# Kernel tuning notes

Measured on AMD Instinct MI355X. Metric: run time of the kernel, lower is better.

Reference implementation:

```python
import jax, jax.numpy as jnp
import numpy as np

# VAR block scales (x,y,z) -> per-scale token counts x*y*z
BLOCK_SCALES = [(1,1,1),(2,2,1),(3,3,1),(4,4,1),(5,5,1),(6,6,1),(8,8,1),(10,10,1),(13,13,1),(16,16,1)]
LENGTHS = [x*y*z for x, y, z in BLOCK_SCALES]  # [1,4,9,...,256], sum = 680
L = int(np.sum(LENGTHS))
B, H, D = 8, 16, 64


def _var_mask():
    # document_id[i] = which scale block token i belongs to
    doc = np.repeat(np.arange(len(LENGTHS), dtype=np.int32), LENGTHS)  # [L]
    idx = np.arange(L)
    same_doc = doc[:, None] == doc[None, :]
    causal = idx[:, None] >= idx[None, :]
    return jnp.asarray(same_doc | causal)  # [L, L] bool


MASK = _var_mask()


def setup_inputs() -> dict:
    key = jax.random.key(0)
    kq, kk, kv = jax.random.split(key, 3)
    q = jax.random.normal(kq, (B, H, L, D), dtype=jnp.float32)
    k = jax.random.normal(kk, (B, H, L, D), dtype=jnp.float32)
    v = jax.random.normal(kv, (B, H, L, D), dtype=jnp.float32)
    return {"q": q, "k": k, "v": v}


def reference(q, k, v):
    # flex_attention default scale = 1/sqrt(head_dim)
    scale = 1.0 / np.sqrt(D).astype(np.float32)
    scores = jnp.einsum("bhqd,bhkd->bhqk", q, k) * scale  # [B,H,L,L]
    neg = jnp.asarray(jnp.finfo(scores.dtype).min, scores.dtype)
    scores = jnp.where(MASK, scores, neg)
    attn = jax.nn.softmax(scores, axis=-1)
    return jnp.einsum("bhqk,bhkd->bhqd", attn, v)
```

## Files before the change

kernel.cpp:

```cpp
#include <hip/hip_runtime.h>


typedef float  f32x4 __attribute__((ext_vector_type(4)));
typedef short  s16x8 __attribute__((ext_vector_type(8)));
typedef unsigned int u32;
typedef u32    u32x4 __attribute__((ext_vector_type(4)));

#define L_TOK 680
#define DHEAD 64
#define NBH   128
#define SCALE_LOG2 0.18033688011112042f

__device__ __forceinline__ int kv_len(int q) {
  return q < 1 ? 1 : q < 5 ? 5 : q < 14 ? 14 : q < 30 ? 30 : q < 55 ? 55
       : q < 91 ? 91 : q < 155 ? 155 : q < 255 ? 255 : q < 424 ? 424 : L_TOK;
}

__device__ __forceinline__ short f2bf(float x) {
  unsigned u = __float_as_uint(x);
  return (short)((u + 0x7FFFu + ((u >> 16) & 1u)) >> 16);
}

__device__ __forceinline__ s16x8 cvt8(f32x4 a, f32x4 b, float sc) {
  s16x8 f;
  f[0] = f2bf(a[0] * sc); f[1] = f2bf(a[1] * sc);
  f[2] = f2bf(a[2] * sc); f[3] = f2bf(a[3] * sc);
  f[4] = f2bf(b[0] * sc); f[5] = f2bf(b[1] * sc);
  f[6] = f2bf(b[2] * sc); f[7] = f2bf(b[3] * sc);
  return f;
}

__device__ __forceinline__ float exp2f_raw(float x) {
  float r; asm("v_exp_f32 %0, %1" : "=v"(r) : "v"(x)); return r;
}
__device__ __forceinline__ u32 cvtpk(float lo, float hi) {
  u32 r; asm("v_cvt_pk_bf16_f32 %0, %1, %2" : "=v"(r) : "v"(lo), "v"(hi)); return r;
}

__global__ __launch_bounds__(512, 4) void var_attn14(
    const float* __restrict__ Qg, const float* __restrict__ Kg,
    const float* __restrict__ Vg, float* __restrict__ Og)
{
  const int tid  = threadIdx.x;
  const int lane = tid & 63, wave = tid >> 6;
  const int l15  = lane & 15, lg = lane >> 4;

  int bid  = blockIdx.x;
  int bhlo = bid & 7;
  int t_   = bid >> 3;
  int qbi  = t_ >> 4;
  int bhhi = t_ & 15;
  int qb2  = (qbi < 3) ? (qbi + 3) : (5 - qbi);
  int bh   = bhhi * 8 + bhlo;
  int qblk = qb2 * 128;

  __shared__ short kbuf[3][64 * DHEAD];
  __shared__ short vbuf[3][64 * DHEAD];

  const int qw        = qblk + wave * 16;
  const int qc        = min(qw + l15, L_TOK - 1);
  const int my_kvlen  = kv_len(qc);
  const int kvmin_w   = kv_len(min(qw, L_TOK - 1));
  const int kv_need_w = (qw < L_TOK) ? kv_len(min(qw + 15, L_TOK - 1)) : 0;
  const int nkv       = kv_len(min(qblk + 127, L_TOK - 1));
  const int nt        = (nkv + 63) >> 6;

  s16x8 qfrag[2];
  {
    const float* qp = Qg + ((size_t)(bh * L_TOK + qc)) * DHEAD + lg * 8;
    #pragma unroll
    for (int ks = 0; ks < 2; ++ks) {
      f32x4 a = *(const f32x4*)(qp + ks * 32);
      f32x4 b = *(const f32x4*)(qp + ks * 32 + 4);
      qfrag[ks] = cvt8(a, b, SCALE_LOG2);
    }
  }

  const float* kbase = Kg + (size_t)bh * L_TOK * DHEAD;
  const float* vbase = Vg + (size_t)bh * L_TOK * DHEAD;

  const int kr_s = tid >> 3, kc_s = tid & 7;
  const int vd_s = tid & 63, lg_s = (tid >> 6) & 3, f_s = tid >> 8;

  f32x4 kA, kB;
  float vA[8];

  auto loadregs = [&](int kt) {
    const int kv0 = kt * 64;
    const float* kp = kbase + (size_t)min(kv0 + kr_s, L_TOK - 1) * DHEAD + kc_s * 8;
    kA = *(const f32x4*)kp;
    kB = *(const f32x4*)(kp + 4);
    #pragma unroll
    for (int i = 0; i < 4; ++i) {
      int kv  = kv0 + f_s * 32 + lg_s * 4 + i;
      vA[i]     = vbase[(size_t)min(kv,      L_TOK - 1) * DHEAD + vd_s];
      vA[4 + i] = vbase[(size_t)min(kv + 16, L_TOK - 1) * DHEAD + vd_s];
    }
  };

  auto writelds = [&](int buf) {
    u32x4 kw;
    kw[0] = cvtpk(kA[0], kA[1]); kw[1] = cvtpk(kA[2], kA[3]);
    kw[2] = cvtpk(kB[0], kB[1]); kw[3] = cvtpk(kB[2], kB[3]);
    *(u32x4*)(&kbuf[buf][kr_s * 64 + ((kc_s ^ (kr_s & 7)) * 8)]) = kw;
    u32x4 vw;
    vw[0] = cvtpk(vA[0], vA[1]); vw[1] = cvtpk(vA[2], vA[3]);
    vw[2] = cvtpk(vA[4], vA[5]); vw[3] = cvtpk(vA[6], vA[7]);
    int pos = (2 * lg_s + f_s) ^ (vd_s & 7);
    *(u32x4*)(&vbuf[buf][vd_s * 64 + pos * 8]) = vw;
  };

  const int swz   = l15 & 7;
  const int koff0 = l15 * 128 + ((lg    ) ^ swz) * 16;
  const int koff1 = l15 * 128 + ((lg + 4) ^ swz) * 16;
  const int voff0 = l15 * 128 + ((2 * lg    ) ^ swz) * 16;
  const int voff1 = l15 * 128 + ((2 * lg + 1) ^ swz) * 16;

  f32x4 oacc[4] = {};
  float l_run = 0.0f;

  loadregs(0);
  writelds(0);
  __syncthreads();

  int bcur = 0;
  for (int kt = 0; kt < nt; ++kt) {
    if (kt + 1 < nt) loadregs(kt + 1);

    const int kv0 = kt * 64;
    if (kv0 < kv_need_w) {
      const char* kb = (const char*)&kbuf[bcur][0];
      const char* vb = (const char*)&vbuf[bcur][0];

      f32x4 sacc[4] = {};
      __builtin_amdgcn_s_setprio(1);
      #pragma unroll
      for (int t16 = 0; t16 < 4; ++t16) {
        s16x8 kf0 = *(const s16x8*)(kb + t16 * 2048 + koff0);
        s16x8 kf1 = *(const s16x8*)(kb + t16 * 2048 + koff1);
        sacc[t16] = __builtin_amdgcn_mfma_f32_16x16x32_bf16(kf0, qfrag[0], sacc[t16], 0, 0, 0);
        sacc[t16] = __builtin_amdgcn_mfma_f32_16x16x32_bf16(kf1, qfrag[1], sacc[t16], 0, 0, 0);
      }
      __builtin_amdgcn_s_setprio(0);

      u32x4 w0, w1;
      float lsum = 0.0f;
      if (kv0 + 64 <= kvmin_w) {
        #pragma unroll
        for (int t16 = 0; t16 < 4; ++t16) {
          float a = exp2f_raw(sacc[t16][0]);
          float b = exp2f_raw(sacc[t16][1]);
          float c = exp2f_raw(sacc[t16][2]);
          float d = exp2f_raw(sacc[t16][3]);
          lsum += (a + b) + (c + d);
          u32 lo = cvtpk(a, b), hi = cvtpk(c, d);
          if (t16 < 2) { w0[2 * t16] = lo; w0[2 * t16 + 1] = hi; }
          else         { w1[2 * (t16 - 2)] = lo; w1[2 * (t16 - 2) + 1] = hi; }
        }
      } else {
        const int kbq = kv0 + lg * 4;
        #pragma unroll
        for (int t16 = 0; t16 < 4; ++t16) {
          float a = (kbq + t16 * 16     < my_kvlen) ? exp2f_raw(sacc[t16][0]) : 0.0f;
          float b = (kbq + t16 * 16 + 1 < my_kvlen) ? exp2f_raw(sacc[t16][1]) : 0.0f;
          float c = (kbq + t16 * 16 + 2 < my_kvlen) ? exp2f_raw(sacc[t16][2]) : 0.0f;
          float d = (kbq + t16 * 16 + 3 < my_kvlen) ? exp2f_raw(sacc[t16][3]) : 0.0f;
          lsum += (a + b) + (c + d);
          u32 lo = cvtpk(a, b), hi = cvtpk(c, d);
          if (t16 < 2) { w0[2 * t16] = lo; w0[2 * t16 + 1] = hi; }
          else         { w1[2 * (t16 - 2)] = lo; w1[2 * (t16 - 2) + 1] = hi; }
        }
      }
      l_run += lsum;
      s16x8 pf0 = __builtin_bit_cast(s16x8, w0);
      s16x8 pf1 = __builtin_bit_cast(s16x8, w1);

      __builtin_amdgcn_s_setprio(1);
      #pragma unroll
      for (int dt = 0; dt < 4; ++dt) {
        s16x8 vf0 = *(const s16x8*)(vb + dt * 2048 + voff0);
        s16x8 vf1 = *(const s16x8*)(vb + dt * 2048 + voff1);
        oacc[dt] = __builtin_amdgcn_mfma_f32_16x16x32_bf16(pf0, vf0, oacc[dt], 0, 0, 0);
        oacc[dt] = __builtin_amdgcn_mfma_f32_16x16x32_bf16(pf1, vf1, oacc[dt], 0, 0, 0);
      }
      __builtin_amdgcn_s_setprio(0);
    }

    if (kt + 1 < nt) {
      int bnext = (bcur == 2) ? 0 : bcur + 1;
      writelds(bnext);
      __syncthreads();
      bcur = bnext;
    }
  }

  l_run += __shfl_xor(l_run, 16);
  l_run += __shfl_xor(l_run, 32);
  float linv = 1.0f / l_run;
  float li_q[4];
  #pragma unroll
  for (int r = 0; r < 4; ++r) li_q[r] = __shfl(linv, lg * 4 + r);
  #pragma unroll
  for (int r = 0; r < 4; ++r) {
    int qo = qw + lg * 4 + r;
    if (qo < L_TOK) {
      float* dst = Og + ((size_t)(bh * L_TOK + qo)) * DHEAD + l15;
      #pragma unroll
      for (int dt = 0; dt < 4; ++dt) dst[dt * 16] = oacc[dt][r] * li_q[r];
    }
  }
}

extern "C" void kernel_launch(void* const* d_in, const int* in_sizes, int n_in,
                              void* d_out, int out_size, void* d_ws, size_t ws_size,
                              hipStream_t stream) {
  const float* q = (const float*)d_in[0];
  const float* k = (const float*)d_in[1];
  const float* v = (const float*)d_in[2];
  float* o = (float*)d_out;
  (void)d_ws; (void)ws_size;
  var_attn14<<<768, 512, 0, stream>>>(q, k, v, o);
}
```

Baseline: 33.16 us.

## Process two 16-row query tiles per wave with 256-thread blocks

Each wave now handles 32 query rows as two 16-row MFMA tiles that share every K and V fragment read from LDS, halving LDS reads per query. The block shrinks from 8 to 4 waves while still covering 128 queries, so each thread stages twice as much K/V into shared memory per tile. This trades lower LDS traffic and fewer waves competing for the barrier against more registers per thread, fewer waves per block, and less latency hiding.

```diff
diff --git a/kernel.cpp b/kernel.cpp
--- a/kernel.cpp
+++ b/kernel.cpp
@@ -37,7 +37,7 @@
   u32 r; asm("v_cvt_pk_bf16_f32 %0, %1, %2" : "=v"(r) : "v"(lo), "v"(hi)); return r;
 }
 
-__global__ __launch_bounds__(512, 4) void var_attn14(
+__global__ __launch_bounds__(256, 3) void var_attn15(
     const float* __restrict__ Qg, const float* __restrict__ Kg,
     const float* __restrict__ Vg, float* __restrict__ Og)
 {
@@ -57,57 +57,72 @@
   __shared__ short kbuf[3][64 * DHEAD];
   __shared__ short vbuf[3][64 * DHEAD];
 
-  const int qw        = qblk + wave * 16;
-  const int qc        = min(qw + l15, L_TOK - 1);
-  const int my_kvlen  = kv_len(qc);
+  const int qw        = qblk + wave * 32;
+  const int q0c       = min(qw + l15,      L_TOK - 1);
+  const int q1c       = min(qw + 16 + l15, L_TOK - 1);
+  const int kvlen0    = kv_len(q0c);
+  const int kvlen1    = kv_len(q1c);
   const int kvmin_w   = kv_len(min(qw, L_TOK - 1));
-  const int kv_need_w = (qw < L_TOK) ? kv_len(min(qw + 15, L_TOK - 1)) : 0;
+  const int kv_need_w = (qw < L_TOK) ? kv_len(min(qw + 31, L_TOK - 1)) : 0;
   const int nkv       = kv_len(min(qblk + 127, L_TOK - 1));
   const int nt        = (nkv + 63) >> 6;
 
-  s16x8 qfrag[2];
+  s16x8 qf0[2], qf1[2];
   {
-    const float* qp = Qg + ((size_t)(bh * L_TOK + qc)) * DHEAD + lg * 8;
+    const float* qp0 = Qg + ((size_t)(bh * L_TOK + q0c)) * DHEAD + lg * 8;
+    const float* qp1 = Qg + ((size_t)(bh * L_TOK + q1c)) * DHEAD + lg * 8;
     #pragma unroll
     for (int ks = 0; ks < 2; ++ks) {
-      f32x4 a = *(const f32x4*)(qp + ks * 32);
-      f32x4 b = *(const f32x4*)(qp + ks * 32 + 4);
-      qfrag[ks] = cvt8(a, b, SCALE_LOG2);
+      f32x4 a0 = *(const f32x4*)(qp0 + ks * 32);
+      f32x4 b0 = *(const f32x4*)(qp0 + ks * 32 + 4);
+      qf0[ks] = cvt8(a0, b0, SCALE_LOG2);
+      f32x4 a1 = *(const f32x4*)(qp1 + ks * 32);
+      f32x4 b1 = *(const f32x4*)(qp1 + ks * 32 + 4);
+      qf1[ks] = cvt8(a1, b1, SCALE_LOG2);
     }
   }
 
   const float* kbase = Kg + (size_t)bh * L_TOK * DHEAD;
   const float* vbase = Vg + (size_t)bh * L_TOK * DHEAD;
 
-  const int kr_s = tid >> 3, kc_s = tid & 7;
-  const int vd_s = tid & 63, lg_s = (tid >> 6) & 3, f_s = tid >> 8;
-
-  f32x4 kA, kB;
-  float vA[8];
+  const int kr_s = tid >> 2, kc_s = tid & 3;
+  const int vd_s = tid & 63, lg_s = tid >> 6;
+
+  f32x4 kA, kB, kC, kD;
+  float vA[16];
 
   auto loadregs = [&](int kt) {
     const int kv0 = kt * 64;
-    const float* kp = kbase + (size_t)min(kv0 + kr_s, L_TOK - 1) * DHEAD + kc_s * 8;
+    const float* kp = kbase + (size_t)min(kv0 + kr_s, L_TOK - 1) * DHEAD + kc_s * 16;
     kA = *(const f32x4*)kp;
     kB = *(const f32x4*)(kp + 4);
+    kC = *(const f32x4*)(kp + 8);
+    kD = *(const f32x4*)(kp + 12);
     #pragma unroll
-    for (int i = 0; i < 4; ++i) {
-      int kv  = kv0 + f_s * 32 + lg_s * 4 + i;
-      vA[i]     = vbase[(size_t)min(kv,      L_TOK - 1) * DHEAD + vd_s];
-      vA[4 + i] = vbase[(size_t)min(kv + 16, L_TOK - 1) * DHEAD + vd_s];
-    }
+    for (int f = 0; f < 2; ++f)
+      #pragma unroll
+      for (int i = 0; i < 4; ++i) {
+        int kv = kv0 + f * 32 + lg_s * 4 + i;
+        vA[f * 8 + i]     = vbase[(size_t)min(kv,      L_TOK - 1) * DHEAD + vd_s];
+        vA[f * 8 + 4 + i] = vbase[(size_t)min(kv + 16, L_TOK - 1) * DHEAD + vd_s];
+      }
   };
 
   auto writelds = [&](int buf) {
-    u32x4 kw;
-    kw[0] = cvtpk(kA[0], kA[1]); kw[1] = cvtpk(kA[2], kA[3]);
-    kw[2] = cvtpk(kB[0], kB[1]); kw[3] = cvtpk(kB[2], kB[3]);
-    *(u32x4*)(&kbuf[buf][kr_s * 64 + ((kc_s ^ (kr_s & 7)) * 8)]) = kw;
-    u32x4 vw;
-    vw[0] = cvtpk(vA[0], vA[1]); vw[1] = cvtpk(vA[2], vA[3]);
-    vw[2] = cvtpk(vA[4], vA[5]); vw[3] = cvtpk(vA[6], vA[7]);
-    int pos = (2 * lg_s + f_s) ^ (vd_s & 7);
-    *(u32x4*)(&vbuf[buf][vd_s * 64 + pos * 8]) = vw;
+    u32x4 k0, k1;
+    k0[0] = cvtpk(kA[0], kA[1]); k0[1] = cvtpk(kA[2], kA[3]);
+    k0[2] = cvtpk(kB[0], kB[1]); k0[3] = cvtpk(kB[2], kB[3]);
+    k1[0] = cvtpk(kC[0], kC[1]); k1[1] = cvtpk(kC[2], kC[3]);
+    k1[2] = cvtpk(kD[0], kD[1]); k1[3] = cvtpk(kD[2], kD[3]);
+    *(u32x4*)(&kbuf[buf][kr_s * 64 + (((2 * kc_s    ) ^ (kr_s & 7)) * 8)]) = k0;
+    *(u32x4*)(&kbuf[buf][kr_s * 64 + (((2 * kc_s + 1) ^ (kr_s & 7)) * 8)]) = k1;
+    u32x4 v0, v1;
+    v0[0] = cvtpk(vA[0],  vA[1]);  v0[1] = cvtpk(vA[2],  vA[3]);
+    v0[2] = cvtpk(vA[4],  vA[5]);  v0[3] = cvtpk(vA[6],  vA[7]);
+    v1[0] = cvtpk(vA[8],  vA[9]);  v1[1] = cvtpk(vA[10], vA[11]);
+    v1[2] = cvtpk(vA[12], vA[13]); v1[3] = cvtpk(vA[14], vA[15]);
+    *(u32x4*)(&vbuf[buf][vd_s * 64 + (((2 * lg_s    ) ^ (vd_s & 7)) * 8)]) = v0;
+    *(u32x4*)(&vbuf[buf][vd_s * 64 + (((2 * lg_s + 1) ^ (vd_s & 7)) * 8)]) = v1;
   };
 
   const int swz   = l15 & 7;
@@ -116,8 +131,8 @@
   const int voff0 = l15 * 128 + ((2 * lg    ) ^ swz) * 16;
   const int voff1 = l15 * 128 + ((2 * lg + 1) ^ swz) * 16;
 
-  f32x4 oacc[4] = {};
-  float l_run = 0.0f;
+  f32x4 o0[4] = {}, o1[4] = {};
+  float l0 = 0.0f, l1 = 0.0f;
 
   loadregs(0);
   writelds(0);
@@ -132,56 +147,88 @@
       const char* kb = (const char*)&kbuf[bcur][0];
       const char* vb = (const char*)&vbuf[bcur][0];
 
-      f32x4 sacc[4] = {};
+      f32x4 s0a[4], s1a[4];
+      #pragma unroll
+      for (int t16 = 0; t16 < 4; ++t16) { s0a[t16] = (f32x4)0; s1a[t16] = (f32x4)0; }
       __builtin_amdgcn_s_setprio(1);
       #pragma unroll
       for (int t16 = 0; t16 < 4; ++t16) {
-        s16x8 kf0 = *(const s16x8*)(kb + t16 * 2048 + koff0);
-        s16x8 kf1 = *(const s16x8*)(kb + t16 * 2048 + koff1);
-        sacc[t16] = __builtin_amdgcn_mfma_f32_16x16x32_bf16(kf0, qfrag[0], sacc[t16], 0, 0, 0);
-        sacc[t16] = __builtin_amdgcn_mfma_f32_16x16x32_bf16(kf1, qfrag[1], sacc[t16], 0, 0, 0);
+        s16x8 kfa = *(const s16x8*)(kb + t16 * 2048 + koff0);
+        s16x8 kfb = *(const s16x8*)(kb + t16 * 2048 + koff1);
+        s0a[t16] = __builtin_amdgcn_mfma_f32_16x16x32_bf16(kfa, qf0[0], s0a[t16], 0, 0, 0);
+        s0a[t16] = __builtin_amdgcn_mfma_f32_16x16x32_bf16(kfb, qf0[1], s0a[t16], 0, 0, 0);
+        s1a[t16] = __builtin_amdgcn_mfma_f32_16x16x32_bf16(kfa, qf1[0], s1a[t16], 0, 0, 0);
+        s1a[t16] = __builtin_amdgcn_mfma_f32_16x16x32_bf16(kfb, qf1[1], s1a[t16], 0, 0, 0);
       }
       __builtin_amdgcn_s_setprio(0);
 
-      u32x4 w0, w1;
-      float lsum = 0.0f;
+      u32x4 w00, w01, w10, w11;
+      float ls0 = 0.0f, ls1 = 0.0f;
       if (kv0 + 64 <= kvmin_w) {
         #pragma unroll
         for (int t16 = 0; t16 < 4; ++t16) {
-          float a = exp2f_raw(sacc[t16][0]);
-          float b = exp2f_raw(sacc[t16][1]);
-          float c = exp2f_raw(sacc[t16][2]);
-          float d = exp2f_raw(sacc[t16][3]);
-          lsum += (a + b) + (c + d);
-          u32 lo = cvtpk(a, b), hi = cvtpk(c, d);
-          if (t16 < 2) { w0[2 * t16] = lo; w0[2 * t16 + 1] = hi; }
-          else         { w1[2 * (t16 - 2)] = lo; w1[2 * (t16 - 2) + 1] = hi; }
+          float a = exp2f_raw(s0a[t16][0]);
+          float b = exp2f_raw(s0a[t16][1]);
+          float c = exp2f_raw(s0a[t16][2]);
+          float d = exp2f_raw(s0a[t16][3]);
+          ls0 += (a + b) + (c + d);
+          u32 lo0 = cvtpk(a, b), hi0 = cvtpk(c, d);
+          float e = exp2f_raw(s1a[t16][0]);
+          float f = exp2f_raw(s1a[t16][1]);
+          float g = exp2f_raw(s1a[t16][2]);
+          float h = exp2f_raw(s1a[t16][3]);
+          ls1 += (e + f) + (g + h);
+          u32 lo1 = cvtpk(e, f), hi1 = cvtpk(g, h);
+          if (t16 < 2) {
+            w00[2 * t16] = lo0; w00[2 * t16 + 1] = hi0;
+            w10[2 * t16] = lo1; w10[2 * t16 + 1] = hi1;
+          } else {
+            w01[2 * (t16 - 2)] = lo0; w01[2 * (t16 - 2) + 1] = hi0;
+            w11[2 * (t16 - 2)] = lo1; w11[2 * (t16 - 2) + 1] = hi1;
+          }
         }
       } else {
         const int kbq = kv0 + lg * 4;
         #pragma unroll
         for (int t16 = 0; t16 < 4; ++t16) {
-          float a = (kbq + t16 * 16     < my_kvlen) ? exp2f_raw(sacc[t16][0]) : 0.0f;
-          float b = (kbq + t16 * 16 + 1 < my_kvlen) ? exp2f_raw(sacc[t16][1]) : 0.0f;
-          float c = (kbq + t16 * 16 + 2 < my_kvlen) ? exp2f_raw(sacc[t16][2]) : 0.0f;
-          float d = (kbq + t16 * 16 + 3 < my_kvlen) ? exp2f_raw(sacc[t16][3]) : 0.0f;
-          lsum += (a + b) + (c + d);
-          u32 lo = cvtpk(a, b), hi = cvtpk(c, d);
-          if (t16 < 2) { w0[2 * t16] = lo; w0[2 * t16 + 1] = hi; }
-          else         { w1[2 * (t16 - 2)] = lo; w1[2 * (t16 - 2) + 1] = hi; }
+          const int k0i = kbq + t16 * 16;
+          float a = (k0i     < kvlen0) ? exp2f_raw(s0a[t16][0]) : 0.0f;
+          float b = (k0i + 1 < kvlen0) ? exp2f_raw(s0a[t16][1]) : 0.0f;
+          float c = (k0i + 2 < kvlen0) ? exp2f_raw(s0a[t16][2]) : 0.0f;
+          float d = (k0i + 3 < kvlen0) ? exp2f_raw(s0a[t16][3]) : 0.0f;
+          ls0 += (a + b) + (c + d);
+          u32 lo0 = cvtpk(a, b), hi0 = cvtpk(c, d);
+          float e = (k0i     < kvlen1) ? exp2f_raw(s1a[t16][0]) : 0.0f;
+          float f = (k0i + 1 < kvlen1) ? exp2f_raw(s1a[t16][1]) : 0.0f;
+          float g = (k0i + 2 < kvlen1) ? exp2f_raw(s1a[t16][2]) : 0.0f;
+          float h = (k0i + 3 < kvlen1) ? exp2f_raw(s1a[t16][3]) : 0.0f;
+          ls1 += (e + f) + (g + h);
+          u32 lo1 = cvtpk(e, f), hi1 = cvtpk(g, h);
+          if (t16 < 2) {
+            w00[2 * t16] = lo0; w00[2 * t16 + 1] = hi0;
+            w10[2 * t16] = lo1; w10[2 * t16 + 1] = hi1;
+          } else {
+            w01[2 * (t16 - 2)] = lo0; w01[2 * (t16 - 2) + 1] = hi0;
+            w11[2 * (t16 - 2)] = lo1; w11[2 * (t16 - 2) + 1] = hi1;
+          }
         }
       }
-      l_run += lsum;
-      s16x8 pf0 = __builtin_bit_cast(s16x8, w0);
-      s16x8 pf1 = __builtin_bit_cast(s16x8, w1);
+      l0 += ls0;
+      l1 += ls1;
+      s16x8 pf00 = __builtin_bit_cast(s16x8, w00);
+      s16x8 pf01 = __builtin_bit_cast(s16x8, w01);
+      s16x8 pf10 = __builtin_bit_cast(s16x8, w10);
+      s16x8 pf11 = __builtin_bit_cast(s16x8, w11);
 
       __builtin_amdgcn_s_setprio(1);
       #pragma unroll
       for (int dt = 0; dt < 4; ++dt) {
         s16x8 vf0 = *(const s16x8*)(vb + dt * 2048 + voff0);
         s16x8 vf1 = *(const s16x8*)(vb + dt * 2048 + voff1);
-        oacc[dt] = __builtin_amdgcn_mfma_f32_16x16x32_bf16(pf0, vf0, oacc[dt], 0, 0, 0);
-        oacc[dt] = __builtin_amdgcn_mfma_f32_16x16x32_bf16(pf1, vf1, oacc[dt], 0, 0, 0);
+        o0[dt] = __builtin_amdgcn_mfma_f32_16x16x32_bf16(pf00, vf0, o0[dt], 0, 0, 0);
+        o0[dt] = __builtin_amdgcn_mfma_f32_16x16x32_bf16(pf01, vf1, o0[dt], 0, 0, 0);
+        o1[dt] = __builtin_amdgcn_mfma_f32_16x16x32_bf16(pf10, vf0, o1[dt], 0, 0, 0);
+        o1[dt] = __builtin_amdgcn_mfma_f32_16x16x32_bf16(pf11, vf1, o1[dt], 0, 0, 0);
       }
       __builtin_amdgcn_s_setprio(0);
     }
@@ -194,19 +241,28 @@
     }
   }
 
-  l_run += __shfl_xor(l_run, 16);
-  l_run += __shfl_xor(l_run, 32);
-  float linv = 1.0f / l_run;
-  float li_q[4];
-  #pragma unroll
-  for (int r = 0; r < 4; ++r) li_q[r] = __shfl(linv, lg * 4 + r);
+  l0 += __shfl_xor(l0, 16); l0 += __shfl_xor(l0, 32);
+  l1 += __shfl_xor(l1, 16); l1 += __shfl_xor(l1, 32);
+  float li0 = 1.0f / l0, li1 = 1.0f / l1;
+  float s0q[4], s1q[4];
   #pragma unroll
   for (int r = 0; r < 4; ++r) {
-    int qo = qw + lg * 4 + r;
-    if (qo < L_TOK) {
-      float* dst = Og + ((size_t)(bh * L_TOK + qo)) * DHEAD + l15;
-      #pragma unroll
-      for (int dt = 0; dt < 4; ++dt) dst[dt * 16] = oacc[dt][r] * li_q[r];
+    s0q[r] = __shfl(li0, lg * 4 + r);
+    s1q[r] = __shfl(li1, lg * 4 + r);
+  }
+  #pragma unroll
+  for (int r = 0; r < 4; ++r) {
+    int qo0 = qw + lg * 4 + r;
+    if (qo0 < L_TOK) {
+      float* dst = Og + ((size_t)(bh * L_TOK + qo0)) * DHEAD + l15;
+      #pragma unroll
+      for (int dt = 0; dt < 4; ++dt) dst[dt * 16] = o0[dt][r] * s0q[r];
+    }
+    int qo1 = qw + 16 + lg * 4 + r;
+    if (qo1 < L_TOK) {
+      float* dst = Og + ((size_t)(bh * L_TOK + qo1)) * DHEAD + l15;
+      #pragma unroll
+      for (int dt = 0; dt < 4; ++dt) dst[dt * 16] = o1[dt][r] * s1q[r];
     }
   }
 }
@@ -219,5 +275,5 @@
   const float* v = (const float*)d_in[2];
   float* o = (float*)d_out;
   (void)d_ws; (void)ws_size;
-  var_attn14<<<768, 512, 0, stream>>>(q, k, v, o);
-}
+  var_attn15<<<768, 256, 0, stream>>>(q, k, v, o);
+}
```

Result: faster. 32.22 us (-2.8%).
